# Kernel tuning notes

Measured on AMD Instinct MI355X. Metric: run time of the kernel, lower is better.

## Reference

```python
import jax, jax.numpy as jnp
import numpy as np

N_NODES = 1000
N_EDGES = 8000
BATCH = 64
IN_DIM = 64
HID = 128
N_CLASSES = 2


def setup_inputs() -> dict:
    key = jax.random.key(0)
    ks = jax.random.split(key, 8)
    x = jax.random.normal(ks[0], (BATCH * N_NODES, IN_DIM), jnp.float32)
    # per-graph random edges, offset so each graph's nodes are disjoint
    ei = jax.random.randint(ks[1], (2, BATCH * N_EDGES), 0, N_NODES)
    offs = jnp.repeat(jnp.arange(BATCH) * N_NODES, N_EDGES)
    edge_index = (ei + offs[None, :]).astype(jnp.int32)
    batch = jnp.repeat(jnp.arange(BATCH), N_NODES).astype(jnp.int32)
    # learnable params (init is ones in source; use uniform [0,1.3] to exercise
    # both the <0.2 zeroing branch and the clamp-at-1 branch)
    edge_weights = jax.random.uniform(ks[2], (N_EDGES,), jnp.float32, 0.0, 1.3)
    node_importance = jax.random.uniform(ks[3], (N_NODES,), jnp.float32, 0.0, 1.3)
    s1 = 1.0 / np.sqrt(IN_DIM)
    W1 = jax.random.uniform(ks[4], (IN_DIM, HID), jnp.float32, -s1, s1)
    b1 = jnp.zeros((HID,), jnp.float32)
    sn = 1.0 / np.sqrt(HID * N_NODES)
    Wn = jax.random.uniform(ks[5], (HID * N_NODES, 32), jnp.float32, -sn, sn)
    bn = jnp.zeros((32,), jnp.float32)
    sc = 1.0 / np.sqrt(32)
    Wc = jax.random.uniform(ks[6], (32, N_CLASSES), jnp.float32, -sc, sc)
    bc = jnp.zeros((N_CLASSES,), jnp.float32)
    return dict(x=x, edge_index=edge_index, batch=batch,
                edge_weights=edge_weights, node_importance=node_importance,
                W1=W1, b1=b1, Wn=Wn, bn=bn, Wc=Wc, bc=bc)


def _gcn(x, src, dst, ew, W, b, n):
    """PyG GCNConv: add self-loops (weight 1), symmetric normalization, linear."""
    loop = jnp.arange(n, dtype=src.dtype)
    src = jnp.concatenate([src, loop])
    dst = jnp.concatenate([dst, loop])
    ew = jnp.concatenate([ew, jnp.ones((n,), ew.dtype)])
    deg = jax.ops.segment_sum(ew, dst, num_segments=n)
    dinv = jnp.where(deg > 0, jax.lax.rsqrt(jnp.maximum(deg, 1e-12)), 0.0)
    norm = dinv[src] * ew * dinv[dst]          # [E+n]
    h = x @ W                                  # [n, HID]
    out = jax.ops.segment_sum(h[src] * norm[:, None], dst, num_segments=n)
    return out + b


def reference(x, edge_index, batch, edge_weights, node_importance,
              W1, b1, Wn, bn, Wc, bc):
    # edge sparsification: zero below 0.2, clamp above at 1
    ew = jnp.where(edge_weights < 0.2, 0.0, jnp.minimum(edge_weights, 1.0))
    ni_clamped = jnp.clip(node_importance, 0.0, 1.0)
    B = edge_index.shape[1] // N_EDGES
    n_total = x.shape[0]
    exp_ew = jnp.tile(ew, B)
    # source uses the RAW (unclamped) node_importance here - replicated
    exp_ni = jnp.tile(node_importance, B)[:, None]
    h = x * exp_ni
    h = _gcn(h, edge_index[0], edge_index[1], exp_ew, W1, b1, n_total)
    h = jax.nn.relu(h)
    # each graph has exactly N_NODES nodes and batch is sorted, so the
    # per-graph mask+pad loop is exactly a reshape
    g = h.reshape(B, N_NODES * h.shape[1])     # [B, N*HID]
    g = g @ Wn + bn                            # [B, 32]
    out = g @ Wc + bc                          # [B, N_CLASSES]
    return (out, ew, ni_clamped)
```

## Files before the change

kernel.cpp:

```cpp
#include <hip/hip_runtime.h>

#define N_NODES_C 1000
#define N_EDGES_C 8000
#define BATCH_C   64
#define IN_DIM_C  64
#define HID_C     128
#define NT (BATCH_C * N_NODES_C)
#define ET (BATCH_C * N_EDGES_C)

#define WS_DEG    0
#define WS_EWS    64000
#define WS_CNT    72000
#define WS_CUR    136000
#define WS_ROWP   200000
#define WS_PEDGE  265536
#define WS_PART2  72000
#define WS_H2     1813824
#define WS_RH     10005824
#define RG_BLOCKS 800

__global__ __launch_bounds__(256) void prep(const float* __restrict__ ew_in,
                                            const float* __restrict__ ni,
                                            float* __restrict__ ws,
                                            float* __restrict__ out) {
    int i = blockIdx.x * 256 + threadIdx.x;
    if (i < NT) {
        ws[WS_DEG + i] = 1.0f;
        ((int*)(ws + WS_CNT))[i] = 0;
    }
    if (i < N_EDGES_C) {
        float w = ew_in[i];
        float s = (w < 0.2f) ? 0.0f : fminf(w, 1.0f);
        ws[WS_EWS + i] = s;
        out[128 + i] = s;
    }
    if (i < N_NODES_C) {
        float v = ni[i];
        out[128 + N_EDGES_C + i] = fminf(fmaxf(v, 0.0f), 1.0f);
    }
}

__global__ __launch_bounds__(256) void deg_cnt(const int* __restrict__ ei,
                                               float* __restrict__ ws) {
    int e = blockIdx.x * 256 + threadIdx.x;
    int d = ei[ET + e];
    int le = e % N_EDGES_C;
    atomicAdd(&ws[WS_DEG + d], ws[WS_EWS + le]);
    atomicAdd(&((int*)(ws + WS_CNT))[d], 1);
}

__global__ __launch_bounds__(256) void csr_scan(float* __restrict__ ws) {
    __shared__ int rs[N_NODES_C + 8];
    __shared__ int wtot[4];
    int g = blockIdx.x, tid = threadIdx.x;
    int lane = tid & 63, wid = tid >> 6;
    int gbase = g * N_NODES_C;
    const int* cnt = (const int*)(ws + WS_CNT) + gbase;

    for (int i = tid; i < N_NODES_C; i += 256)
        ws[WS_DEG + gbase + i] = rsqrtf(ws[WS_DEG + gbase + i]);

    int s0 = 0, s1 = 0, s2 = 0, s3 = 0, tsum = 0;
    if (tid < 250) {
        s0 = cnt[4 * tid]; s1 = cnt[4 * tid + 1];
        s2 = cnt[4 * tid + 2]; s3 = cnt[4 * tid + 3];
        tsum = s0 + s1 + s2 + s3;
    }
    int v = tsum;
    #pragma unroll
    for (int off = 1; off < 64; off <<= 1) {
        int n = __shfl_up(v, off, 64);
        if (lane >= off) v += n;
    }
    if (lane == 63) wtot[wid] = v;
    __syncthreads();
    int base = 0;
    for (int w = 0; w < wid; ++w) base += wtot[w];
    int excl = base + v - tsum;
    if (tid < 250) {
        rs[4 * tid]     = excl;
        rs[4 * tid + 1] = excl + s0;
        rs[4 * tid + 2] = excl + s0 + s1;
        rs[4 * tid + 3] = excl + s0 + s1 + s2;
    }
    if (tid == 255) rs[N_NODES_C] = N_EDGES_C;
    __syncthreads();

    int* rowp = (int*)(ws + WS_ROWP) + g * 1024;
    int* cur  = (int*)(ws + WS_CUR) + gbase;
    for (int i = tid; i <= N_NODES_C; i += 256) rowp[i] = rs[i];
    for (int i = tid; i < N_NODES_C; i += 256) cur[i] = rs[i];
}

__global__ __launch_bounds__(256) void scatter(const int* __restrict__ ei,
                                               float* __restrict__ ws) {
    int e = blockIdx.x * 256 + threadIdx.x;
    int g = e / N_EDGES_C;
    int le = e - g * N_EDGES_C;
    int s = ei[e];
    int d = ei[ET + e];
    const float* dinv = ws + WS_DEG;
    float nm = dinv[s] * ws[WS_EWS + le] * dinv[d];
    int pos = atomicAdd(&((int*)(ws + WS_CUR))[d], 1);
    ((int2*)(ws + WS_PEDGE))[g * N_EDGES_C + pos] =
        make_int2(s, __float_as_int(nm));
}

__global__ __launch_bounds__(256) void gemm_h2(const float* __restrict__ x,
                                               const float* __restrict__ ni,
                                               const float* __restrict__ W1,
                                               float* __restrict__ h2) {
    __shared__ float xs[128][65];
    __shared__ float wsm[64 * 128];
    int tid = threadIdx.x;
    int base = blockIdx.x * 128;

    #pragma unroll
    for (int i = 0; i < 8; ++i) {
        int idx = i * 1024 + tid * 4;
        int r = idx >> 6, d = idx & 63;
        float4 v = *(const float4*)&x[(base + r) * 64 + d];
        float s = ni[(base + r) % N_NODES_C];
        xs[r][d + 0] = v.x * s;
        xs[r][d + 1] = v.y * s;
        xs[r][d + 2] = v.z * s;
        xs[r][d + 3] = v.w * s;
    }
    #pragma unroll
    for (int i = 0; i < 8; ++i) {
        int idx = i * 1024 + tid * 4;
        *(float4*)&wsm[idx] = *(const float4*)&W1[idx];
    }
    __syncthreads();

    int tx = tid & 15, ty = tid >> 4;
    int r0 = ty * 8, c0 = tx * 8;
    float acc[8][8];
    #pragma unroll
    for (int i = 0; i < 8; ++i)
        #pragma unroll
        for (int j = 0; j < 8; ++j) acc[i][j] = 0.0f;

    for (int d = 0; d < 64; ++d) {
        float a[8];
        #pragma unroll
        for (int i = 0; i < 8; ++i) a[i] = xs[r0 + i][d];
        float4 b0 = *(float4*)&wsm[d * 128 + c0];
        float4 b1 = *(float4*)&wsm[d * 128 + c0 + 4];
        float b[8] = {b0.x, b0.y, b0.z, b0.w, b1.x, b1.y, b1.z, b1.w};
        #pragma unroll
        for (int i = 0; i < 8; ++i)
            #pragma unroll
            for (int j = 0; j < 8; ++j)
                acc[i][j] = fmaf(a[i], b[j], acc[i][j]);
    }

    #pragma unroll
    for (int i = 0; i < 8; ++i) {
        float* dst = &h2[(base + r0 + i) * HID_C + c0];
        float4 o0 = {acc[i][0], acc[i][1], acc[i][2], acc[i][3]};
        float4 o1 = {acc[i][4], acc[i][5], acc[i][6], acc[i][7]};
        *(float4*)dst = o0;
        *(float4*)(dst + 4) = o1;
    }
}

__global__ __launch_bounds__(256) void spmm_op(const float* __restrict__ ws_ro,
                                               const float* __restrict__ h2,
                                               const float* __restrict__ b1,
                                               float* __restrict__ rh) {
    int bid = blockIdx.x;
    int g = bid & 63, slice = bid >> 6;
    int t = threadIdx.x;
    if (t >= 250) return;
    int p = slice * 250 + t;
    int dst = p >> 3, chunk = p & 7, c0 = chunk << 4;

    const int*  rowp  = (const int*)(ws_ro + WS_ROWP) + g * 1024;
    const int2* pedge = (const int2*)(ws_ro + WS_PEDGE) + g * N_EDGES_C;
    const float* dinv = ws_ro + WS_DEG;

    int e0 = rowp[dst], e1 = rowp[dst + 1];
    float4 a0 = {0,0,0,0}, a1 = {0,0,0,0}, a2 = {0,0,0,0}, a3 = {0,0,0,0};
    for (int e = e0; e < e1; ++e) {
        int2 ed = pedge[e];
        float nm = __int_as_float(ed.y);
        const float* hp = &h2[ed.x * HID_C + c0];
        float4 h0 = *(const float4*)(hp + 0);
        float4 h1 = *(const float4*)(hp + 4);
        float4 h2v = *(const float4*)(hp + 8);
        float4 h3 = *(const float4*)(hp + 12);
        a0.x = fmaf(h0.x, nm, a0.x); a0.y = fmaf(h0.y, nm, a0.y);
        a0.z = fmaf(h0.z, nm, a0.z); a0.w = fmaf(h0.w, nm, a0.w);
        a1.x = fmaf(h1.x, nm, a1.x); a1.y = fmaf(h1.y, nm, a1.y);
        a1.z = fmaf(h1.z, nm, a1.z); a1.w = fmaf(h1.w, nm, a1.w);
        a2.x = fmaf(h2v.x, nm, a2.x); a2.y = fmaf(h2v.y, nm, a2.y);
        a2.z = fmaf(h2v.z, nm, a2.z); a2.w = fmaf(h2v.w, nm, a2.w);
        a3.x = fmaf(h3.x, nm, a3.x); a3.y = fmaf(h3.y, nm, a3.y);
        a3.z = fmaf(h3.z, nm, a3.z); a3.w = fmaf(h3.w, nm, a3.w);
    }

    int node = g * N_NODES_C + dst;
    float dv = dinv[node], dv2 = dv * dv;
    const float* sp = &h2[node * HID_C + c0];
    float* op = &rh[node * HID_C + c0];
    #pragma unroll
    for (int q = 0; q < 4; ++q) {
        float4 sv = *(const float4*)(sp + q * 4);
        float4 bv = *(const float4*)&b1[c0 + q * 4];
        float4 av = q == 0 ? a0 : q == 1 ? a1 : q == 2 ? a2 : a3;
        float4 o;
        o.x = fmaxf(fmaf(sv.x, dv2, av.x) + bv.x, 0.0f);
        o.y = fmaxf(fmaf(sv.y, dv2, av.y) + bv.y, 0.0f);
        o.z = fmaxf(fmaf(sv.z, dv2, av.z) + bv.z, 0.0f);
        o.w = fmaxf(fmaf(sv.w, dv2, av.w) + bv.w, 0.0f);
        *(float4*)(op + q * 4) = o;
    }
}

__global__ __launch_bounds__(1024) void spmm_ip(const float* __restrict__ ws_ro,
                                                float* __restrict__ h2,
                                                const float* __restrict__ b1) {
    __shared__ float res[N_NODES_C * 16];
    int bid = blockIdx.x;
    int g  = bid & 63;
    int c0 = (bid >> 6) * 16;
    int tid = threadIdx.x;
    int fq = tid & 3, dslot = tid >> 2;

    const int*  rowp  = (const int*)(ws_ro + WS_ROWP) + g * 1024;
    const int2* pedge = (const int2*)(ws_ro + WS_PEDGE) + g * N_EDGES_C;
    const float* dinv = ws_ro + WS_DEG;
    int gbase = g * N_NODES_C;

    for (int iter = 0; iter < 4; ++iter) {
        int d = iter * 256 + dslot;
        if (d < N_NODES_C) {
            int e0 = rowp[d], e1 = rowp[d + 1];
            float4 a = make_float4(0.f, 0.f, 0.f, 0.f);
            for (int e = e0; e < e1; ++e) {
                int2 ed = pedge[e];
                float nm = __int_as_float(ed.y);
                float4 hv = *(const float4*)&h2[ed.x * HID_C + c0 + fq * 4];
                a.x = fmaf(hv.x, nm, a.x);
                a.y = fmaf(hv.y, nm, a.y);
                a.z = fmaf(hv.z, nm, a.z);
                a.w = fmaf(hv.w, nm, a.w);
            }
            *(float4*)&res[d * 16 + fq * 4] = a;
        }
    }
    __syncthreads();

    for (int idx = tid; idx < N_NODES_C * 16; idx += 1024) {
        int v = idx >> 4, f = idx & 15;
        int node = gbase + v;
        float dv = dinv[node];
        float val = res[idx] + h2[node * HID_C + c0 + f] * (dv * dv) + b1[c0 + f];
        h2[node * HID_C + c0 + f] = fmaxf(val, 0.0f);
    }
}

__global__ __launch_bounds__(256) void reduce_g(const float* __restrict__ rh,
                                                const float* __restrict__ Wn,
                                                float* __restrict__ part) {
    int tid = threadIdx.x;
    int j = tid & 31, bg = tid >> 5;
    int k0 = blockIdx.x * 160;
    float acc[8] = {0, 0, 0, 0, 0, 0, 0, 0};
    for (int kk = 0; kk < 160; kk += 8) {
        int k = k0 + kk;
        float w[8];
        #pragma unroll
        for (int q = 0; q < 8; ++q) w[q] = Wn[(k + q) * 32 + j];
        #pragma unroll
        for (int u = 0; u < 8; ++u) {
            const float* rp = &rh[(bg * 8 + u) * 128000 + k];
            float4 r0 = *(const float4*)(rp + 0);
            float4 r1 = *(const float4*)(rp + 4);
            acc[u] = fmaf(r0.x, w[0], acc[u]);
            acc[u] = fmaf(r0.y, w[1], acc[u]);
            acc[u] = fmaf(r0.z, w[2], acc[u]);
            acc[u] = fmaf(r0.w, w[3], acc[u]);
            acc[u] = fmaf(r1.x, w[4], acc[u]);
            acc[u] = fmaf(r1.y, w[5], acc[u]);
            acc[u] = fmaf(r1.z, w[6], acc[u]);
            acc[u] = fmaf(r1.w, w[7], acc[u]);
        }
    }
    #pragma unroll
    for (int u = 0; u < 8; ++u)
        part[blockIdx.x * 2048 + (bg * 8 + u) * 32 + j] = acc[u];
}

__global__ __launch_bounds__(256) void final_out(const float* __restrict__ ws_ro,
                                                 const float* __restrict__ bn,
                                                 const float* __restrict__ Wc,
                                                 const float* __restrict__ bc,
                                                 float* __restrict__ out) {
    __shared__ float red[256];
    int g = blockIdx.x;
    int tid = threadIdx.x;
    int j = tid & 31, cl = tid >> 5;
    const float* part = ws_ro + WS_PART2;
    float s = 0.0f;
    for (int c = cl; c < RG_BLOCKS; c += 8)
        s += part[c * 2048 + g * 32 + j];
    red[tid] = s;
    __syncthreads();
    if (tid < 32) {
        float gv = red[tid];
        #pragma unroll
        for (int q = 1; q < 8; ++q) gv += red[q * 32 + tid];
        gv += bn[tid];
        float o0 = gv * Wc[tid * 2 + 0];
        float o1 = gv * Wc[tid * 2 + 1];
        #pragma unroll
        for (int off = 16; off >= 1; off >>= 1) {
            o0 += __shfl_xor(o0, off);
            o1 += __shfl_xor(o1, off);
        }
        if (tid == 0) {
            out[g * 2 + 0] = o0 + bc[0];
            out[g * 2 + 1] = o1 + bc[1];
        }
    }
}

extern "C" void kernel_launch(void* const* d_in, const int* in_sizes, int n_in,
                              void* d_out, int out_size, void* d_ws, size_t ws_size,
                              hipStream_t stream) {
    const float* x  = (const float*)d_in[0];
    const int*   ei = (const int*)d_in[1];
    const float* ew = (const float*)d_in[3];
    const float* ni = (const float*)d_in[4];
    const float* W1 = (const float*)d_in[5];
    const float* b1 = (const float*)d_in[6];
    const float* Wn = (const float*)d_in[7];
    const float* bn = (const float*)d_in[8];
    const float* Wc = (const float*)d_in[9];
    const float* bc = (const float*)d_in[10];
    float* out = (float*)d_out;
    float* ws  = (float*)d_ws;

    bool big = ws_size >= (size_t)(WS_RH + 8192000) * sizeof(float);
    float* h2 = ws + WS_H2;
    float* rh = big ? ws + WS_RH : h2;

    prep<<<NT / 256, 256, 0, stream>>>(ew, ni, ws, out);
    gemm_h2<<<NT / 128, 256, 0, stream>>>(x, ni, W1, h2);
    deg_cnt<<<ET / 256, 256, 0, stream>>>(ei, ws);
    csr_scan<<<BATCH_C, 256, 0, stream>>>(ws);
    scatter<<<ET / 256, 256, 0, stream>>>(ei, ws);
    if (big)
        spmm_op<<<BATCH_C * 32, 256, 0, stream>>>(ws, h2, b1, rh);
    else
        spmm_ip<<<BATCH_C * 8, 1024, 0, stream>>>(ws, h2, b1);
    reduce_g<<<RG_BLOCKS, 256, 0, stream>>>(rh, Wn, ws + WS_PART2);
    final_out<<<BATCH_C, 256, 0, stream>>>(ws, bn, Wc, bc, out);
}
```

Before: 274.0 us.

## Pack degree and count into one 64-bit atomic, stage Wn in LDS

The degree and edge-count accumulation is merged into a single 64-bit atomic per edge. The weight is stored as 16.16 fixed point in the low half and the count in the high half, and the buffer is zeroed with a memset instead of a prep kernel. reduce_g now stages its Wn chunk in shared memory, and the big-workspace path uses smaller chunks with more blocks (1600) to raise parallelism. Fixed-point quantisation of edge weights slightly changes degree precision, and the partial sums now go to the h2 region.

```diff
diff --git a/kernel.cpp b/kernel.cpp
--- a/kernel.cpp
+++ b/kernel.cpp
@@ -10,24 +10,18 @@
 
 #define WS_DEG    0
 #define WS_EWS    64000
-#define WS_CNT    72000
-#define WS_CUR    136000
+#define WS_PCK    72000
 #define WS_ROWP   200000
 #define WS_PEDGE  265536
 #define WS_PART2  72000
 #define WS_H2     1813824
 #define WS_RH     10005824
-#define RG_BLOCKS 800
 
 __global__ __launch_bounds__(256) void prep(const float* __restrict__ ew_in,
                                             const float* __restrict__ ni,
                                             float* __restrict__ ws,
                                             float* __restrict__ out) {
     int i = blockIdx.x * 256 + threadIdx.x;
-    if (i < NT) {
-        ws[WS_DEG + i] = 1.0f;
-        ((int*)(ws + WS_CNT))[i] = 0;
-    }
     if (i < N_EDGES_C) {
         float w = ew_in[i];
         float s = (w < 0.2f) ? 0.0f : fminf(w, 1.0f);
@@ -44,26 +38,34 @@
                                                float* __restrict__ ws) {
     int e = blockIdx.x * 256 + threadIdx.x;
     int d = ei[ET + e];
-    int le = e % N_EDGES_C;
-    atomicAdd(&ws[WS_DEG + d], ws[WS_EWS + le]);
-    atomicAdd(&((int*)(ws + WS_CNT))[d], 1);
+    float w = ws[WS_EWS + e % N_EDGES_C];
+    unsigned long long pk =
+        (1ull << 32) | (unsigned)(w * 65536.0f + 0.5f);
+    atomicAdd((unsigned long long*)(ws + WS_PCK) + d, pk);
 }
 
 __global__ __launch_bounds__(256) void csr_scan(float* __restrict__ ws) {
+    __shared__ int cntl[N_NODES_C];
     __shared__ int rs[N_NODES_C + 8];
     __shared__ int wtot[4];
     int g = blockIdx.x, tid = threadIdx.x;
     int lane = tid & 63, wid = tid >> 6;
     int gbase = g * N_NODES_C;
-    const int* cnt = (const int*)(ws + WS_CNT) + gbase;
-
-    for (int i = tid; i < N_NODES_C; i += 256)
-        ws[WS_DEG + gbase + i] = rsqrtf(ws[WS_DEG + gbase + i]);
+    const unsigned long long* pck =
+        (const unsigned long long*)(ws + WS_PCK) + gbase;
+
+    for (int i = tid; i < N_NODES_C; i += 256) {
+        unsigned long long p = pck[i];
+        cntl[i] = (int)(p >> 32);
+        float deg = 1.0f + (float)(unsigned)p * (1.0f / 65536.0f);
+        ws[WS_DEG + gbase + i] = rsqrtf(deg);
+    }
+    __syncthreads();
 
     int s0 = 0, s1 = 0, s2 = 0, s3 = 0, tsum = 0;
     if (tid < 250) {
-        s0 = cnt[4 * tid]; s1 = cnt[4 * tid + 1];
-        s2 = cnt[4 * tid + 2]; s3 = cnt[4 * tid + 3];
+        s0 = cntl[4 * tid]; s1 = cntl[4 * tid + 1];
+        s2 = cntl[4 * tid + 2]; s3 = cntl[4 * tid + 3];
         tsum = s0 + s1 + s2 + s3;
     }
     int v = tsum;
@@ -87,7 +89,7 @@
     __syncthreads();
 
     int* rowp = (int*)(ws + WS_ROWP) + g * 1024;
-    int* cur  = (int*)(ws + WS_CUR) + gbase;
+    int* cur  = (int*)(ws + WS_PCK) + gbase;
     for (int i = tid; i <= N_NODES_C; i += 256) rowp[i] = rs[i];
     for (int i = tid; i < N_NODES_C; i += 256) cur[i] = rs[i];
 }
@@ -101,7 +103,7 @@
     int d = ei[ET + e];
     const float* dinv = ws + WS_DEG;
     float nm = dinv[s] * ws[WS_EWS + le] * dinv[d];
-    int pos = atomicAdd(&((int*)(ws + WS_CUR))[d], 1);
+    int pos = atomicAdd((int*)(ws + WS_PCK) + d, 1);
     ((int2*)(ws + WS_PEDGE))[g * N_EDGES_C + pos] =
         make_int2(s, __float_as_int(nm));
 }
@@ -261,21 +263,26 @@
     }
 }
 
+template<int CHUNK>
 __global__ __launch_bounds__(256) void reduce_g(const float* __restrict__ rh,
                                                 const float* __restrict__ Wn,
                                                 float* __restrict__ part) {
+    __shared__ float wn[CHUNK * 32];
     int tid = threadIdx.x;
+    int k0 = blockIdx.x * CHUNK;
+    for (int idx = tid * 4; idx < CHUNK * 32; idx += 1024)
+        *(float4*)&wn[idx] = *(const float4*)&Wn[k0 * 32 + idx];
+    __syncthreads();
+
     int j = tid & 31, bg = tid >> 5;
-    int k0 = blockIdx.x * 160;
     float acc[8] = {0, 0, 0, 0, 0, 0, 0, 0};
-    for (int kk = 0; kk < 160; kk += 8) {
-        int k = k0 + kk;
+    for (int kk = 0; kk < CHUNK; kk += 8) {
         float w[8];
         #pragma unroll
-        for (int q = 0; q < 8; ++q) w[q] = Wn[(k + q) * 32 + j];
+        for (int q = 0; q < 8; ++q) w[q] = wn[(kk + q) * 32 + j];
         #pragma unroll
         for (int u = 0; u < 8; ++u) {
-            const float* rp = &rh[(bg * 8 + u) * 128000 + k];
+            const float* rp = &rh[(bg * 8 + u) * 128000 + k0 + kk];
             float4 r0 = *(const float4*)(rp + 0);
             float4 r1 = *(const float4*)(rp + 4);
             acc[u] = fmaf(r0.x, w[0], acc[u]);
@@ -293,18 +300,18 @@
         part[blockIdx.x * 2048 + (bg * 8 + u) * 32 + j] = acc[u];
 }
 
-__global__ __launch_bounds__(256) void final_out(const float* __restrict__ ws_ro,
+__global__ __launch_bounds__(256) void final_out(const float* __restrict__ part,
                                                  const float* __restrict__ bn,
                                                  const float* __restrict__ Wc,
                                                  const float* __restrict__ bc,
-                                                 float* __restrict__ out) {
+                                                 float* __restrict__ out,
+                                                 int nchunks) {
     __shared__ float red[256];
     int g = blockIdx.x;
     int tid = threadIdx.x;
     int j = tid & 31, cl = tid >> 5;
-    const float* part = ws_ro + WS_PART2;
     float s = 0.0f;
-    for (int c = cl; c < RG_BLOCKS; c += 8)
+    for (int c = cl; c < nchunks; c += 8)
         s += part[c * 2048 + g * 32 + j];
     red[tid] = s;
     __syncthreads();
@@ -347,15 +354,19 @@
     float* h2 = ws + WS_H2;
     float* rh = big ? ws + WS_RH : h2;
 
-    prep<<<NT / 256, 256, 0, stream>>>(ew, ni, ws, out);
+    hipMemsetAsync(ws + WS_PCK, 0, 64000 * sizeof(unsigned long long), stream);
+    prep<<<32, 256, 0, stream>>>(ew, ni, ws, out);
     gemm_h2<<<NT / 128, 256, 0, stream>>>(x, ni, W1, h2);
     deg_cnt<<<ET / 256, 256, 0, stream>>>(ei, ws);
     csr_scan<<<BATCH_C, 256, 0, stream>>>(ws);
     scatter<<<ET / 256, 256, 0, stream>>>(ei, ws);
-    if (big)
+    if (big) {
         spmm_op<<<BATCH_C * 32, 256, 0, stream>>>(ws, h2, b1, rh);
-    else
+        reduce_g<80><<<1600, 256, 0, stream>>>(rh, Wn, ws + WS_H2);
+        final_out<<<BATCH_C, 256, 0, stream>>>(ws + WS_H2, bn, Wc, bc, out, 1600);
+    } else {
         spmm_ip<<<BATCH_C * 8, 1024, 0, stream>>>(ws, h2, b1);
-    reduce_g<<<RG_BLOCKS, 256, 0, stream>>>(rh, Wn, ws + WS_PART2);
-    final_out<<<BATCH_C, 256, 0, stream>>>(ws, bn, Wc, bc, out);
-}
+        reduce_g<160><<<800, 256, 0, stream>>>(rh, Wn, ws + WS_PART2);
+        final_out<<<BATCH_C, 256, 0, stream>>>(ws + WS_PART2, bn, Wc, bc, out, 800);
+    }
+}
```

After: 289.0 us. 5.5% more time.
